# Kernel optimization log

Measured on AMD Instinct MI355X. Metric: run time of the kernel, lower is better.

The kernel has to match this reference:

```python
import jax, jax.numpy as jnp
import numpy as np

DIM = 768
HEADS = 12
DIM_HEAD = 64
INNER = HEADS * DIM_HEAD  # 768
SCALE = DIM_HEAD ** -0.5


def setup_inputs() -> dict:
    key = jax.random.key(0)
    k1, k2, k3, k4 = jax.random.split(key, 4)
    x = jax.random.normal(k1, (4, 1024, DIM), dtype=jnp.float32)
    # nn.Linear weights stored as [out, in]; we keep [in, out] for x @ W.
    w_qkv = jax.random.normal(k2, (DIM, 3 * INNER), dtype=jnp.float32) * (DIM ** -0.5)
    w_out = jax.random.normal(k3, (INNER, DIM), dtype=jnp.float32) * (INNER ** -0.5)
    b_out = jax.random.normal(k4, (DIM,), dtype=jnp.float32) * 0.02
    return {"x": x, "w_qkv": w_qkv, "w_out": w_out, "b_out": b_out}


def reference(x, w_qkv, w_out, b_out):
    B, N, _ = x.shape
    qkv = x @ w_qkv  # [B, N, 3*inner]
    q, k, v = jnp.split(qkv, 3, axis=-1)
    # b n (h d) -> b h n d
    def to_heads(t):
        return t.reshape(B, N, HEADS, DIM_HEAD).transpose(0, 2, 1, 3)
    q, k, v = to_heads(q), to_heads(k), to_heads(v)
    dots = jnp.einsum('bhnd,bhmd->bhnm', q, k) * SCALE  # [B, H, N, N]
    attn = jax.nn.softmax(dots, axis=-1)  # dropout p=0 -> identity
    out = jnp.einsum('bhnm,bhmd->bhnd', attn, v)
    out = out.transpose(0, 2, 1, 3).reshape(B, N, INNER)  # b h n d -> b n (h d)
    return out @ w_out + b_out
```

## Files before the change

### kernel.cpp

```cpp
#include <hip/hip_runtime.h>
#include <math.h>


typedef __attribute__((ext_vector_type(8))) __bf16 bf16x8;
typedef __attribute__((ext_vector_type(4))) float f32x4;
typedef __attribute__((ext_vector_type(16))) float f32x16;
typedef unsigned short u16;
typedef unsigned int u32;

#define ZERO16 {0,0,0,0,0,0,0,0,0,0,0,0,0,0,0,0}

__device__ __forceinline__ u16 f2bf(float f) {
    union { float f; unsigned u; } v; v.f = f;
    unsigned r = v.u + 0x7FFF + ((v.u >> 16) & 1);
    return (u16)(r >> 16);
}

__device__ __forceinline__ u32 cvtpk(float lo, float hi) {
    u32 r;
    asm("v_cvt_pk_bf16_f32 %0, %1, %2" : "=v"(r) : "v"(lo), "v"(hi));
    return r;
}
__device__ __forceinline__ float xhalf_max(float x) {
    float o = __shfl_xor(x, 32);
    return fmaxf(x, o);
}
__device__ __forceinline__ float xhalf_sum(float x) {
    float o = __shfl_xor(x, 32);
    return x + o;
}

__global__ __launch_bounds__(256) void prep(const float* __restrict__ x,
                                            const float* __restrict__ w_qkv,
                                            const float* __restrict__ w_out,
                                            u16* __restrict__ xb,
                                            u16* __restrict__ wqkvT,
                                            u16* __restrict__ woutT) {
    __shared__ float T[32][33];
    const int bid = blockIdx.x;
    if (bid < 3072) {
        int i = bid * 256 + threadIdx.x;
        float4 v = reinterpret_cast<const float4*>(x)[i];
        union { u16 s[4]; int2 p; } o;
        o.s[0] = f2bf(v.x); o.s[1] = f2bf(v.y); o.s[2] = f2bf(v.z); o.s[3] = f2bf(v.w);
        reinterpret_cast<int2*>(xb)[i] = o.p;
        return;
    }
    const float* in;
    u16* out;
    int R, C, c0, r0;
    if (bid < 4800) {
        int r = bid - 3072;
        in = w_qkv; out = wqkvT; R = 768; C = 2304;
        c0 = (r % 72) * 32; r0 = (r / 72) * 32;
    } else {
        int r = bid - 4800;
        in = w_out; out = woutT; R = 768; C = 768;
        c0 = (r % 24) * 32; r0 = (r / 24) * 32;
    }
    const int tx = threadIdx.x & 31;
    const int ty = threadIdx.x >> 5;
#pragma unroll
    for (int p = 0; p < 4; ++p) {
        int ry = ty + p * 8;
        T[ry][tx] = in[(size_t)(r0 + ry) * C + c0 + tx];
    }
    __syncthreads();
#pragma unroll
    for (int p = 0; p < 4; ++p) {
        int cy = ty + p * 8;
        out[(size_t)(c0 + cy) * R + r0 + tx] = f2bf(T[tx][cy]);
    }
}

__global__ __launch_bounds__(256) void gemm_qkv(const u16* __restrict__ A,
                                                const u16* __restrict__ BT,
                                                u16* __restrict__ Qf,
                                                u16* __restrict__ Kf,
                                                u16* __restrict__ Vf) {
    __shared__ u16 As[2][64 * 32];
    __shared__ u16 Bs[2][128 * 32];
    const int tid = threadIdx.x;
    const int lane = tid & 63;
    const int w = tid >> 6;
    const int wm = w >> 1, wn = w & 1;
    const int lr = lane & 15;
    const int lk = lane >> 4;
    const int orig = blockIdx.x >> 3;
    const int xcd = blockIdx.x & 7;
    const int col0 = (orig >> 3) * 128;
    const int row0 = (xcd * 8 + (orig & 7)) * 64;
    const int sr = lane >> 2;
    const int scg = lane & 3;

    f32x4 acc[2][4];
#pragma unroll
    for (int mi = 0; mi < 2; ++mi)
#pragma unroll
        for (int nj = 0; nj < 4; ++nj) acc[mi][nj] = (f32x4){0.f, 0.f, 0.f, 0.f};

    const u16* aSrc = A  + (size_t)(row0 + w * 16 + sr) * 768 + scg * 8;
    const u16* bSrc0 = BT + (size_t)(col0 + w * 16 + sr) * 768 + scg * 8;
    const u16* bSrc1 = BT + (size_t)(col0 + (4 + w) * 16 + sr) * 768 + scg * 8;
    u16* aDst = &As[0][(w * 16 + sr) * 32 + scg * 8];
    u16* bDst0 = &Bs[0][(w * 16 + sr) * 32 + scg * 8];
    u16* bDst1 = &Bs[0][((4 + w) * 16 + sr) * 32 + scg * 8];

#define LOADR(RA, RB0, RB1, K0)                                         \
    RA  = *reinterpret_cast<const int4*>(aSrc  + (K0));                 \
    RB0 = *reinterpret_cast<const int4*>(bSrc0 + (K0));                 \
    RB1 = *reinterpret_cast<const int4*>(bSrc1 + (K0));
#define WRITER(BUF, RA, RB0, RB1)                                       \
    *reinterpret_cast<int4*>(aDst  + (BUF) * 64 * 32)  = RA;            \
    *reinterpret_cast<int4*>(bDst0 + (BUF) * 128 * 32) = RB0;           \
    *reinterpret_cast<int4*>(bDst1 + (BUF) * 128 * 32) = RB1;
#define COMPUTE(BUF)                                                          \
    {                                                                         \
        bf16x8 af[2], bfr[4];                                                 \
        _Pragma("unroll")                                                     \
        for (int mi = 0; mi < 2; ++mi)                                        \
            af[mi] = *reinterpret_cast<const bf16x8*>(&As[BUF][(wm * 32 + mi * 16 + lr) * 32 + lk * 8]); \
        _Pragma("unroll")                                                     \
        for (int nj = 0; nj < 4; ++nj)                                        \
            bfr[nj] = *reinterpret_cast<const bf16x8*>(&Bs[BUF][(wn * 64 + nj * 16 + lr) * 32 + lk * 8]); \
        __builtin_amdgcn_s_setprio(1);                                        \
        _Pragma("unroll")                                                     \
        for (int mi = 0; mi < 2; ++mi)                                        \
            _Pragma("unroll")                                                 \
            for (int nj = 0; nj < 4; ++nj)                                    \
                acc[mi][nj] = __builtin_amdgcn_mfma_f32_16x16x32_bf16(af[mi], bfr[nj], acc[mi][nj], 0, 0, 0); \
        __builtin_amdgcn_s_setprio(0);                                        \
    }
#define BARRIER()                                                       \
    asm volatile("s_waitcnt lgkmcnt(0)" ::: "memory");                  \
    __builtin_amdgcn_sched_barrier(0);                                  \
    __builtin_amdgcn_s_barrier();

    int4 rA_a, rA_b0, rA_b1, rB_a, rB_b0, rB_b1;
    LOADR(rA_a, rA_b0, rA_b1, 0);
    LOADR(rB_a, rB_b0, rB_b1, 32);
    WRITER(0, rA_a, rA_b0, rA_b1);
    BARRIER();

#pragma unroll 1
    for (int t = 0; t < 24; t += 2) {
        if (t + 2 < 24) { LOADR(rA_a, rA_b0, rA_b1, (t + 2) * 32); }
        COMPUTE(0);
        WRITER(1, rB_a, rB_b0, rB_b1);
        BARRIER();
        if (t + 3 < 24) { LOADR(rB_a, rB_b0, rB_b1, (t + 3) * 32); }
        COMPUTE(1);
        if (t + 2 < 24) { WRITER(0, rA_a, rA_b0, rA_b1); }
        BARRIER();
    }
#undef LOADR
#undef WRITER
#undef COMPUTE
#undef BARRIER

    const int which = col0 / 768;
    const int cb = col0 - which * 768;
#pragma unroll
    for (int mi = 0; mi < 2; ++mi) {
#pragma unroll
        for (int i = 0; i < 4; ++i) {
            int r = row0 + wm * 32 + mi * 16 + lk * 4 + i;
            int b = r >> 10, n = r & 1023;
#pragma unroll
            for (int nj = 0; nj < 4; ++nj) {
                int cw = cb + wn * 64 + nj * 16 + lr;
                int h = cw >> 6, d = cw & 63;
                int bh = b * 12 + h;
                float val = acc[mi][nj][i];
                if (which == 2) {
                    size_t off = ((((size_t)bh * 16 + (n >> 6)) * 4 + ((n >> 4) & 3)) * 2 + ((n >> 3) & 1)) * 512
                                 + d * 8 + (n & 7);
                    Vf[off] = f2bf(val);
                } else {
                    size_t off = ((((size_t)bh * 32 + (n >> 5)) * 4 + (d >> 4)) * 2 + ((d >> 3) & 1)) * 256
                                 + (n & 31) * 8 + (d & 7);
                    if (which == 0) Qf[off] = f2bf(val * 0.18033688f);
                    else            Kf[off] = f2bf(val);
                }
            }
        }
    }
}

#define GETO(dt, r) ((dt) == 0 ? o0[r] : o1[r])

__global__ __launch_bounds__(256) void attn_mfma(const u16* __restrict__ Qf,
                                                 const u16* __restrict__ Kf,
                                                 const u16* __restrict__ Vf,
                                                 u16* __restrict__ attn_out) {
    __shared__ float OtM[2][64][33];
    __shared__ float Lm[2][32], Ll[2][32];
    __shared__ u16 Os[2][32][72];

    const int tid = threadIdx.x;
    const int lane = tid & 63;
    const int w = tid >> 6;
    const int qsub = w & 1;
    const int half = w >> 1;
    const int l31 = lane & 31;
    const int hi = lane >> 5;

    const int bid = blockIdx.x;
    const int lin = (bid & 7) * 96 + (bid >> 3);
    const int qt = lin & 15;
    const int bh = lin >> 4;

    const u16* Qh = Qf + (size_t)bh * 65536;
    const u16* Kh = Kf + (size_t)bh * 65536;
    const u16* Vh = Vf + (size_t)bh * 65536;

    bf16x8 qf[4];
#pragma unroll
    for (int kt = 0; kt < 4; ++kt)
        qf[kt] = *reinterpret_cast<const bf16x8*>(
            Qh + (((size_t)(qt * 2 + qsub) * 4 + kt) * 2 + hi) * 256 + l31 * 8);

    f32x16 o0 = ZERO16, o1 = ZERO16;
    float m = -1e30f, l = 0.f;

    for (int it = 0; it < 8; ++it) {
        const int kb0 = it * 4 + half * 2;
        const int kvb = it * 2 + half;

        bf16x8 kf0[4], kf1[4];
#pragma unroll
        for (int kt = 0; kt < 4; ++kt) {
            kf0[kt] = *reinterpret_cast<const bf16x8*>(
                Kh + (((size_t)kb0 * 4 + kt) * 2 + hi) * 256 + l31 * 8);
            kf1[kt] = *reinterpret_cast<const bf16x8*>(
                Kh + (((size_t)(kb0 + 1) * 4 + kt) * 2 + hi) * 256 + l31 * 8);
        }
        bf16x8 vf0[4], vf1[4];
#pragma unroll
        for (int ks = 0; ks < 4; ++ks) {
            const u16* vb = Vh + (((size_t)kvb * 4 + ks) * 2 + hi) * 512;
            vf0[ks] = *reinterpret_cast<const bf16x8*>(vb + l31 * 8);
            vf1[ks] = *reinterpret_cast<const bf16x8*>(vb + (l31 + 32) * 8);
        }

        f32x16 s0 = ZERO16, s1 = ZERO16;
        __builtin_amdgcn_s_setprio(1);
#pragma unroll
        for (int kt = 0; kt < 4; ++kt) s0 = __builtin_amdgcn_mfma_f32_32x32x16_bf16(kf0[kt], qf[kt], s0, 0, 0, 0);
#pragma unroll
        for (int kt = 0; kt < 4; ++kt) s1 = __builtin_amdgcn_mfma_f32_32x32x16_bf16(kf1[kt], qf[kt], s1, 0, 0, 0);
        __builtin_amdgcn_s_setprio(0);

        float mx[8];
#pragma unroll
        for (int i = 0; i < 8; ++i)
            mx[i] = fmaxf(fmaxf(s0[2*i], s0[2*i+1]), fmaxf(s1[2*i], s1[2*i+1]));
        float pmax = fmaxf(fmaxf(fmaxf(mx[0], mx[1]), fmaxf(mx[2], mx[3])),
                           fmaxf(fmaxf(mx[4], mx[5]), fmaxf(mx[6], mx[7])));
        pmax = xhalf_max(pmax);

        if (!__all(pmax <= m + 8.f)) {
            float mn = fmaxf(m, pmax);
            float c = __builtin_amdgcn_exp2f(m - mn);
            m = mn; l *= c;
            o0 = o0 * c; o1 = o1 * c;
        }

#pragma unroll
        for (int r = 0; r < 16; ++r) s0[r] = __builtin_amdgcn_exp2f(s0[r] - m);
#pragma unroll
        for (int r = 0; r < 16; ++r) s1[r] = __builtin_amdgcn_exp2f(s1[r] - m);
        float sm[8];
#pragma unroll
        for (int i = 0; i < 8; ++i)
            sm[i] = (s0[2*i] + s0[2*i+1]) + (s1[2*i] + s1[2*i+1]);
        float tsum = ((sm[0]+sm[1]) + (sm[2]+sm[3])) + ((sm[4]+sm[5]) + (sm[6]+sm[7]));
        l += xhalf_sum(tsum);

        bf16x8 pb[4];
#define PACK_GROUP(S, G, OUT)                                           \
        {                                                               \
            u32 X0 = cvtpk(S[8*(G)+0], S[8*(G)+1]);                     \
            u32 X1 = cvtpk(S[8*(G)+2], S[8*(G)+3]);                     \
            u32 Y0 = cvtpk(S[8*(G)+4], S[8*(G)+5]);                     \
            u32 Y1 = cvtpk(S[8*(G)+6], S[8*(G)+7]);                     \
            u32 X0s = (u32)__shfl_xor((int)X0, 32);                     \
            u32 X1s = (u32)__shfl_xor((int)X1, 32);                     \
            u32 Y0s = (u32)__shfl_xor((int)Y0, 32);                     \
            u32 Y1s = (u32)__shfl_xor((int)Y1, 32);                     \
            union { u32 u[4]; bf16x8 v; } pk_;                          \
            pk_.u[0] = hi ? Y0s : X0;                                   \
            pk_.u[1] = hi ? Y1s : X1;                                   \
            pk_.u[2] = hi ? Y0 : X0s;                                   \
            pk_.u[3] = hi ? Y1 : X1s;                                   \
            OUT = pk_.v;                                                \
        }
        PACK_GROUP(s0, 0, pb[0]);
        PACK_GROUP(s0, 1, pb[1]);
        PACK_GROUP(s1, 0, pb[2]);
        PACK_GROUP(s1, 1, pb[3]);
#undef PACK_GROUP

        __builtin_amdgcn_s_setprio(1);
#pragma unroll
        for (int ks = 0; ks < 4; ++ks) {
            o0 = __builtin_amdgcn_mfma_f32_32x32x16_bf16(vf0[ks], pb[ks], o0, 0, 0, 0);
            o1 = __builtin_amdgcn_mfma_f32_32x32x16_bf16(vf1[ks], pb[ks], o1, 0, 0, 0);
        }
        __builtin_amdgcn_s_setprio(0);
    }

    if (half == 1) {
#pragma unroll
        for (int dt = 0; dt < 2; ++dt)
#pragma unroll
            for (int r = 0; r < 16; ++r)
                OtM[qsub][dt * 32 + (r & 3) + 8 * (r >> 2) + 4 * hi][l31] = GETO(dt, r);
        Lm[qsub][l31] = m;
        Ll[qsub][l31] = l;
    }
    __syncthreads();
    if (half == 0) {
        float m2 = Lm[qsub][l31], l2 = Ll[qsub][l31];
        float mn = fmaxf(m, m2);
        float a = __builtin_amdgcn_exp2f(m - mn);
        float bsc = __builtin_amdgcn_exp2f(m2 - mn);
        float lm = l * a + l2 * bsc;
        float inv = 1.0f / lm;
        float av = a * inv, bv = bsc * inv;
#pragma unroll
        for (int dt = 0; dt < 2; ++dt)
#pragma unroll
            for (int rq = 0; rq < 4; ++rq) {
                int d0 = dt * 32 + 8 * rq + 4 * hi;
                float v0 = GETO(dt, rq * 4 + 0) * av + OtM[qsub][d0 + 0][l31] * bv;
                float v1 = GETO(dt, rq * 4 + 1) * av + OtM[qsub][d0 + 1][l31] * bv;
                float v2 = GETO(dt, rq * 4 + 2) * av + OtM[qsub][d0 + 2][l31] * bv;
                float v3 = GETO(dt, rq * 4 + 3) * av + OtM[qsub][d0 + 3][l31] * bv;
                uint2 pr;
                pr.x = cvtpk(v0, v1);
                pr.y = cvtpk(v2, v3);
                *reinterpret_cast<uint2*>(&Os[qsub][l31][d0]) = pr;
            }
    }
    __syncthreads();

    const int b = bh / 12, h = bh % 12;
#pragma unroll
    for (int it2 = 0; it2 < 2; ++it2) {
        int idx = tid + it2 * 256;
        int token = idx >> 3;
        int chunk = idx & 7;
        int4 v = *reinterpret_cast<const int4*>(&Os[token >> 5][token & 31][chunk * 8]);
        *reinterpret_cast<int4*>(&attn_out[((size_t)(b * 1024 + qt * 64 + token)) * 768 + h * 64 + chunk * 8]) = v;
    }
}

__global__ __launch_bounds__(256) void gemm_out(const u16* __restrict__ A,
                                                const u16* __restrict__ BT,
                                                const float* __restrict__ bias,
                                                float* __restrict__ out) {
    __shared__ u16 As[2][64 * 32];
    __shared__ u16 Bs[2][128 * 32];
    const int tid = threadIdx.x;
    const int lane = tid & 63;
    const int w = tid >> 6;
    const int wm = w >> 1, wn = w & 1;
    const int lr = lane & 15;
    const int lk = lane >> 4;
    const int orig = blockIdx.x >> 3;
    const int xcd = blockIdx.x & 7;
    const int col0 = (orig >> 3) * 128;
    const int row0 = (xcd * 8 + (orig & 7)) * 64;
    const int sr = lane >> 2;
    const int scg = lane & 3;

    f32x4 acc[2][4];
#pragma unroll
    for (int mi = 0; mi < 2; ++mi)
#pragma unroll
        for (int nj = 0; nj < 4; ++nj) acc[mi][nj] = (f32x4){0.f, 0.f, 0.f, 0.f};

    const u16* aSrc = A  + (size_t)(row0 + w * 16 + sr) * 768 + scg * 8;
    const u16* bSrc0 = BT + (size_t)(col0 + w * 16 + sr) * 768 + scg * 8;
    const u16* bSrc1 = BT + (size_t)(col0 + (4 + w) * 16 + sr) * 768 + scg * 8;
    u16* aDst = &As[0][(w * 16 + sr) * 32 + scg * 8];
    u16* bDst0 = &Bs[0][(w * 16 + sr) * 32 + scg * 8];
    u16* bDst1 = &Bs[0][((4 + w) * 16 + sr) * 32 + scg * 8];

#define LOADR(RA, RB0, RB1, K0)                                         \
    RA  = *reinterpret_cast<const int4*>(aSrc  + (K0));                 \
    RB0 = *reinterpret_cast<const int4*>(bSrc0 + (K0));                 \
    RB1 = *reinterpret_cast<const int4*>(bSrc1 + (K0));
#define WRITER(BUF, RA, RB0, RB1)                                       \
    *reinterpret_cast<int4*>(aDst  + (BUF) * 64 * 32)  = RA;            \
    *reinterpret_cast<int4*>(bDst0 + (BUF) * 128 * 32) = RB0;           \
    *reinterpret_cast<int4*>(bDst1 + (BUF) * 128 * 32) = RB1;
#define COMPUTE(BUF)                                                          \
    {                                                                         \
        bf16x8 af[2], bfr[4];                                                 \
        _Pragma("unroll")                                                     \
        for (int mi = 0; mi < 2; ++mi)                                        \
            af[mi] = *reinterpret_cast<const bf16x8*>(&As[BUF][(wm * 32 + mi * 16 + lr) * 32 + lk * 8]); \
        _Pragma("unroll")                                                     \
        for (int nj = 0; nj < 4; ++nj)                                        \
            bfr[nj] = *reinterpret_cast<const bf16x8*>(&Bs[BUF][(wn * 64 + nj * 16 + lr) * 32 + lk * 8]); \
        __builtin_amdgcn_s_setprio(1);                                        \
        _Pragma("unroll")                                                     \
        for (int mi = 0; mi < 2; ++mi)                                        \
            _Pragma("unroll")                                                 \
            for (int nj = 0; nj < 4; ++nj)                                    \
                acc[mi][nj] = __builtin_amdgcn_mfma_f32_16x16x32_bf16(af[mi], bfr[nj], acc[mi][nj], 0, 0, 0); \
        __builtin_amdgcn_s_setprio(0);                                        \
    }
#define BARRIER()                                                       \
    asm volatile("s_waitcnt lgkmcnt(0)" ::: "memory");                  \
    __builtin_amdgcn_sched_barrier(0);                                  \
    __builtin_amdgcn_s_barrier();

    int4 rA_a, rA_b0, rA_b1, rB_a, rB_b0, rB_b1;
    LOADR(rA_a, rA_b0, rA_b1, 0);
    LOADR(rB_a, rB_b0, rB_b1, 32);
    WRITER(0, rA_a, rA_b0, rA_b1);
    BARRIER();

#pragma unroll 1
    for (int t = 0; t < 24; t += 2) {
        if (t + 2 < 24) { LOADR(rA_a, rA_b0, rA_b1, (t + 2) * 32); }
        COMPUTE(0);
        WRITER(1, rB_a, rB_b0, rB_b1);
        BARRIER();
        if (t + 3 < 24) { LOADR(rB_a, rB_b0, rB_b1, (t + 3) * 32); }
        COMPUTE(1);
        if (t + 2 < 24) { WRITER(0, rA_a, rA_b0, rA_b1); }
        BARRIER();
    }
#undef LOADR
#undef WRITER
#undef COMPUTE
#undef BARRIER

#pragma unroll
    for (int mi = 0; mi < 2; ++mi)
#pragma unroll
        for (int i = 0; i < 4; ++i) {
            int r = row0 + wm * 32 + mi * 16 + lk * 4 + i;
#pragma unroll
            for (int nj = 0; nj < 4; ++nj) {
                int c = col0 + wn * 64 + nj * 16 + lr;
                out[(size_t)r * 768 + c] = acc[mi][nj][i] + bias[c];
            }
        }
}

extern "C" void kernel_launch(void* const* d_in, const int* in_sizes, int n_in,
                              void* d_out, int out_size, void* d_ws, size_t ws_size,
                              hipStream_t stream) {
    const float* x     = (const float*)d_in[0];
    const float* w_qkv = (const float*)d_in[1];
    const float* w_out = (const float*)d_in[2];
    const float* b_out = (const float*)d_in[3];
    float* out = (float*)d_out;

    u16* ws = (u16*)d_ws;
    const size_t n_x = (size_t)4096 * 768;
    u16* xb     = ws;
    u16* wqkvT  = xb + n_x;
    u16* woutT  = wqkvT + (size_t)2304 * 768;
    u16* Qfr    = woutT + (size_t)768 * 768;
    u16* Kfr    = Qfr + n_x;
    u16* Vfr    = Kfr + n_x;
    u16* attnb  = Vfr + n_x;

    prep<<<5376, 256, 0, stream>>>(x, w_qkv, w_out, xb, wqkvT, woutT);
    gemm_qkv<<<1152, 256, 0, stream>>>(xb, wqkvT, Qfr, Kfr, Vfr);
    attn_mfma<<<768, 256, 0, stream>>>(Qfr, Kfr, Vfr, attnb);
    gemm_out<<<384, 256, 0, stream>>>(attnb, woutT, b_out, out);
}
```

Baseline: 83.81 us.

## Fuse x bf16 conversion into QKV GEMM, deepen prefetch, remap block tiles

Removes the separate fp32→bf16 conversion of x from the prep kernel; the QKV GEMM now loads fp32 x directly and converts with v_cvt_pk_bf16_f32 while staging into LDS. Both GEMMs switch to a three-deep register prefetch ring with a fully unrolled k-loop. The QKV block-to-tile mapping is changed so each XCD covers a 16-row by 9-column group, aiming for better L2 reuse. This saves a kernel pass over x and a workspace round trip, but doubles A-tile global bytes in the GEMM and raises register pressure.

```diff
diff --git a/kernel.cpp b/kernel.cpp
--- a/kernel.cpp
+++ b/kernel.cpp
@@ -30,31 +30,20 @@
     return x + o;
 }
 
-__global__ __launch_bounds__(256) void prep(const float* __restrict__ x,
-                                            const float* __restrict__ w_qkv,
+__global__ __launch_bounds__(256) void prep(const float* __restrict__ w_qkv,
                                             const float* __restrict__ w_out,
-                                            u16* __restrict__ xb,
                                             u16* __restrict__ wqkvT,
                                             u16* __restrict__ woutT) {
     __shared__ float T[32][33];
     const int bid = blockIdx.x;
-    if (bid < 3072) {
-        int i = bid * 256 + threadIdx.x;
-        float4 v = reinterpret_cast<const float4*>(x)[i];
-        union { u16 s[4]; int2 p; } o;
-        o.s[0] = f2bf(v.x); o.s[1] = f2bf(v.y); o.s[2] = f2bf(v.z); o.s[3] = f2bf(v.w);
-        reinterpret_cast<int2*>(xb)[i] = o.p;
-        return;
-    }
     const float* in;
     u16* out;
     int R, C, c0, r0;
-    if (bid < 4800) {
-        int r = bid - 3072;
+    if (bid < 1728) {
         in = w_qkv; out = wqkvT; R = 768; C = 2304;
-        c0 = (r % 72) * 32; r0 = (r / 72) * 32;
+        c0 = (bid % 72) * 32; r0 = (bid / 72) * 32;
     } else {
-        int r = bid - 4800;
+        int r = bid - 1728;
         in = w_out; out = woutT; R = 768; C = 768;
         c0 = (r % 24) * 32; r0 = (r / 24) * 32;
     }
@@ -73,7 +62,7 @@
     }
 }
 
-__global__ __launch_bounds__(256) void gemm_qkv(const u16* __restrict__ A,
+__global__ __launch_bounds__(256) void gemm_qkv(const float* __restrict__ X,
                                                 const u16* __restrict__ BT,
                                                 u16* __restrict__ Qf,
                                                 u16* __restrict__ Kf,
@@ -86,10 +75,10 @@
     const int wm = w >> 1, wn = w & 1;
     const int lr = lane & 15;
     const int lk = lane >> 4;
-    const int orig = blockIdx.x >> 3;
     const int xcd = blockIdx.x & 7;
-    const int col0 = (orig >> 3) * 128;
-    const int row0 = (xcd * 8 + (orig & 7)) * 64;
+    const int lid = blockIdx.x >> 3;
+    const int row0 = ((xcd & 3) * 16 + (lid & 15)) * 64;
+    const int col0 = ((xcd >> 2) * 9 + (lid >> 4)) * 128;
     const int sr = lane >> 2;
     const int scg = lane & 3;
 
@@ -99,21 +88,32 @@
 #pragma unroll
         for (int nj = 0; nj < 4; ++nj) acc[mi][nj] = (f32x4){0.f, 0.f, 0.f, 0.f};
 
-    const u16* aSrc = A  + (size_t)(row0 + w * 16 + sr) * 768 + scg * 8;
+    const float* aSrc = X + (size_t)(row0 + w * 16 + sr) * 768 + scg * 8;
     const u16* bSrc0 = BT + (size_t)(col0 + w * 16 + sr) * 768 + scg * 8;
     const u16* bSrc1 = BT + (size_t)(col0 + (4 + w) * 16 + sr) * 768 + scg * 8;
     u16* aDst = &As[0][(w * 16 + sr) * 32 + scg * 8];
     u16* bDst0 = &Bs[0][(w * 16 + sr) * 32 + scg * 8];
     u16* bDst1 = &Bs[0][((4 + w) * 16 + sr) * 32 + scg * 8];
 
-#define LOADR(RA, RB0, RB1, K0)                                         \
-    RA  = *reinterpret_cast<const int4*>(aSrc  + (K0));                 \
-    RB0 = *reinterpret_cast<const int4*>(bSrc0 + (K0));                 \
-    RB1 = *reinterpret_cast<const int4*>(bSrc1 + (K0));
-#define WRITER(BUF, RA, RB0, RB1)                                       \
-    *reinterpret_cast<int4*>(aDst  + (BUF) * 64 * 32)  = RA;            \
-    *reinterpret_cast<int4*>(bDst0 + (BUF) * 128 * 32) = RB0;           \
-    *reinterpret_cast<int4*>(bDst1 + (BUF) * 128 * 32) = RB1;
+    float4 sa0[3], sa1[3];
+    int4 sb0[3], sb1[3];
+
+#define LOADR(S, K0)                                                    \
+    sa0[S] = *reinterpret_cast<const float4*>(aSrc + (K0));             \
+    sa1[S] = *reinterpret_cast<const float4*>(aSrc + (K0) + 4);         \
+    sb0[S] = *reinterpret_cast<const int4*>(bSrc0 + (K0));              \
+    sb1[S] = *reinterpret_cast<const int4*>(bSrc1 + (K0));
+#define WRITER(BUF, S)                                                  \
+    {                                                                   \
+        int4 av;                                                        \
+        av.x = (int)cvtpk(sa0[S].x, sa0[S].y);                          \
+        av.y = (int)cvtpk(sa0[S].z, sa0[S].w);                          \
+        av.z = (int)cvtpk(sa1[S].x, sa1[S].y);                          \
+        av.w = (int)cvtpk(sa1[S].z, sa1[S].w);                          \
+        *reinterpret_cast<int4*>(aDst  + (BUF) * 64 * 32)  = av;        \
+        *reinterpret_cast<int4*>(bDst0 + (BUF) * 128 * 32) = sb0[S];    \
+        *reinterpret_cast<int4*>(bDst1 + (BUF) * 128 * 32) = sb1[S];    \
+    }
 #define COMPUTE(BUF)                                                          \
     {                                                                         \
         bf16x8 af[2], bfr[4];                                                 \
@@ -136,22 +136,18 @@
     __builtin_amdgcn_sched_barrier(0);                                  \
     __builtin_amdgcn_s_barrier();
 
-    int4 rA_a, rA_b0, rA_b1, rB_a, rB_b0, rB_b1;
-    LOADR(rA_a, rA_b0, rA_b1, 0);
-    LOADR(rB_a, rB_b0, rB_b1, 32);
-    WRITER(0, rA_a, rA_b0, rA_b1);
+    LOADR(0, 0);
+    LOADR(1, 32);
+    LOADR(2, 64);
+    WRITER(0, 0);
     BARRIER();
 
-#pragma unroll 1
-    for (int t = 0; t < 24; t += 2) {
-        if (t + 2 < 24) { LOADR(rA_a, rA_b0, rA_b1, (t + 2) * 32); }
-        COMPUTE(0);
-        WRITER(1, rB_a, rB_b0, rB_b1);
-        BARRIER();
-        if (t + 3 < 24) { LOADR(rB_a, rB_b0, rB_b1, (t + 3) * 32); }
-        COMPUTE(1);
-        if (t + 2 < 24) { WRITER(0, rA_a, rA_b0, rA_b1); }
-        BARRIER();
+#pragma unroll
+    for (int t = 0; t < 24; ++t) {
+        if (t + 3 < 24) { LOADR(t % 3, (t + 3) * 32); }
+        COMPUTE(t & 1);
+        if (t + 1 < 24) { WRITER((t + 1) & 1, (t + 1) % 3); }
+        if (t + 1 < 24) { BARRIER(); }
     }
 #undef LOADR
 #undef WRITER
@@ -368,10 +364,10 @@
     const int wm = w >> 1, wn = w & 1;
     const int lr = lane & 15;
     const int lk = lane >> 4;
-    const int orig = blockIdx.x >> 3;
     const int xcd = blockIdx.x & 7;
-    const int col0 = (orig >> 3) * 128;
-    const int row0 = (xcd * 8 + (orig & 7)) * 64;
+    const int lid = blockIdx.x >> 3;
+    const int row0 = (xcd * 8 + (lid & 7)) * 64;
+    const int col0 = (lid >> 3) * 128;
     const int sr = lane >> 2;
     const int scg = lane & 3;
 
@@ -388,14 +384,16 @@
     u16* bDst0 = &Bs[0][(w * 16 + sr) * 32 + scg * 8];
     u16* bDst1 = &Bs[0][((4 + w) * 16 + sr) * 32 + scg * 8];
 
-#define LOADR(RA, RB0, RB1, K0)                                         \
-    RA  = *reinterpret_cast<const int4*>(aSrc  + (K0));                 \
-    RB0 = *reinterpret_cast<const int4*>(bSrc0 + (K0));                 \
-    RB1 = *reinterpret_cast<const int4*>(bSrc1 + (K0));
-#define WRITER(BUF, RA, RB0, RB1)                                       \
-    *reinterpret_cast<int4*>(aDst  + (BUF) * 64 * 32)  = RA;            \
-    *reinterpret_cast<int4*>(bDst0 + (BUF) * 128 * 32) = RB0;           \
-    *reinterpret_cast<int4*>(bDst1 + (BUF) * 128 * 32) = RB1;
+    int4 sa[3], sb0[3], sb1[3];
+
+#define LOADR(S, K0)                                                    \
+    sa[S]  = *reinterpret_cast<const int4*>(aSrc  + (K0));              \
+    sb0[S] = *reinterpret_cast<const int4*>(bSrc0 + (K0));              \
+    sb1[S] = *reinterpret_cast<const int4*>(bSrc1 + (K0));
+#define WRITER(BUF, S)                                                  \
+    *reinterpret_cast<int4*>(aDst  + (BUF) * 64 * 32)  = sa[S];         \
+    *reinterpret_cast<int4*>(bDst0 + (BUF) * 128 * 32) = sb0[S];        \
+    *reinterpret_cast<int4*>(bDst1 + (BUF) * 128 * 32) = sb1[S];
 #define COMPUTE(BUF)                                                          \
     {                                                                         \
         bf16x8 af[2], bfr[4];                                                 \
@@ -418,22 +416,18 @@
     __builtin_amdgcn_sched_barrier(0);                                  \
     __builtin_amdgcn_s_barrier();
 
-    int4 rA_a, rA_b0, rA_b1, rB_a, rB_b0, rB_b1;
-    LOADR(rA_a, rA_b0, rA_b1, 0);
-    LOADR(rB_a, rB_b0, rB_b1, 32);
-    WRITER(0, rA_a, rA_b0, rA_b1);
+    LOADR(0, 0);
+    LOADR(1, 32);
+    LOADR(2, 64);
+    WRITER(0, 0);
     BARRIER();
 
-#pragma unroll 1
-    for (int t = 0; t < 24; t += 2) {
-        if (t + 2 < 24) { LOADR(rA_a, rA_b0, rA_b1, (t + 2) * 32); }
-        COMPUTE(0);
-        WRITER(1, rB_a, rB_b0, rB_b1);
-        BARRIER();
-        if (t + 3 < 24) { LOADR(rB_a, rB_b0, rB_b1, (t + 3) * 32); }
-        COMPUTE(1);
-        if (t + 2 < 24) { WRITER(0, rA_a, rA_b0, rA_b1); }
-        BARRIER();
+#pragma unroll
+    for (int t = 0; t < 24; ++t) {
+        if (t + 3 < 24) { LOADR(t % 3, (t + 3) * 32); }
+        COMPUTE(t & 1);
+        if (t + 1 < 24) { WRITER((t + 1) & 1, (t + 1) % 3); }
+        if (t + 1 < 24) { BARRIER(); }
     }
 #undef LOADR
 #undef WRITER
@@ -464,16 +458,15 @@
 
     u16* ws = (u16*)d_ws;
     const size_t n_x = (size_t)4096 * 768;
-    u16* xb     = ws;
-    u16* wqkvT  = xb + n_x;
+    u16* wqkvT  = ws;
     u16* woutT  = wqkvT + (size_t)2304 * 768;
     u16* Qfr    = woutT + (size_t)768 * 768;
     u16* Kfr    = Qfr + n_x;
     u16* Vfr    = Kfr + n_x;
     u16* attnb  = Vfr + n_x;
 
-    prep<<<5376, 256, 0, stream>>>(x, w_qkv, w_out, xb, wqkvT, woutT);
-    gemm_qkv<<<1152, 256, 0, stream>>>(xb, wqkvT, Qfr, Kfr, Vfr);
+    prep<<<2304, 256, 0, stream>>>(w_qkv, w_out, wqkvT, woutT);
+    gemm_qkv<<<1152, 256, 0, stream>>>(x, wqkvT, Qfr, Kfr, Vfr);
     attn_mfma<<<768, 256, 0, stream>>>(Qfr, Kfr, Vfr, attnb);
     gemm_out<<<384, 256, 0, stream>>>(attnb, woutT, b_out, out);
 }
```

After: 92.71 us. +10.6%, slower.
